# Performance work log

Hardware: AMD Instinct MI355X
Metric: run time of the kernel (lower is better)

## Reference

```python
import jax, jax.numpy as jnp
import numpy as np

B, Q, LE, D, P, A = 8, 32, 128, 512, 32, 128


def setup_inputs() -> dict:
    key = jax.random.key(0)
    ks = jax.random.split(key, 8)
    exp_tokens = jax.random.normal(ks[0], (B, Q, LE, D), dtype=jnp.float32)
    exp_mask = jax.random.randint(ks[1], (B, Q, LE), 0, 2, dtype=jnp.int32)
    s_j = jax.random.normal(ks[2], (B, P, D), dtype=jnp.float32)
    req_mask = jax.random.randint(ks[3], (B, P), 0, 2, dtype=jnp.int32)
    sc = 1.0 / np.sqrt(D)
    Ws_w = jax.random.normal(ks[4], (A, D), dtype=jnp.float32) * sc
    Ws_b = jax.random.normal(ks[5], (A,), dtype=jnp.float32) * 0.01
    U_w = jax.random.normal(ks[6], (A, D), dtype=jnp.float32) * sc
    v_w = jax.random.normal(ks[7], (1, A), dtype=jnp.float32) * (1.0 / np.sqrt(A))
    return {"exp_tokens": exp_tokens, "exp_mask": exp_mask, "s_j": s_j,
            "req_mask": req_mask, "Ws_w": Ws_w, "Ws_b": Ws_b, "U_w": U_w, "v_w": v_w}


def reference(exp_tokens, exp_mask, s_j, req_mask, Ws_w, Ws_b, U_w, v_w):
    # ws: (B,P,A); uh: (B,Q,Le,A)
    ws = jnp.einsum('bpd,ad->bpa', s_j, Ws_w) + Ws_b
    uh = jnp.einsum('bqtd,ad->bqta', exp_tokens, U_w)
    # broadcast add -> (B,Q,P,Le,A), tanh, project with v -> (B,Q,P,Le)
    scored = jnp.tanh(uh[:, :, None, :, :] + ws[:, None, :, None, :])
    e = jnp.einsum('bqpta,a->bqpt', scored, v_w[0])
    tok_mask = exp_mask[:, :, None, :]  # (B,Q,1,Le) broadcast over P
    e = jnp.where(tok_mask == 0, jnp.float32(-1e9), e)
    # joint softmax over Q*Le per (b,p)
    e_t = jnp.transpose(e, (0, 2, 1, 3)).reshape(e.shape[0], e.shape[2], -1)
    a = jax.nn.softmax(e_t, axis=-1).reshape(e.shape[0], e.shape[2], e.shape[1], e.shape[3])
    a = jnp.transpose(a, (0, 2, 1, 3))  # (B,Q,P,Le)
    s_rlk = jnp.einsum('bqpt,bqtd->bqpd', a, exp_tokens)
    rmask = req_mask[:, None, :, None].astype(s_rlk.dtype)
    return s_rlk * rmask
```

## Files before the change

### kernel.cpp

```cpp
#include <hip/hip_runtime.h>
#include <hip/hip_bf16.h>

#define B_  8
#define Q_  32
#define LE_ 128
#define D_  512
#define P_  32
#define A_  128

typedef __attribute__((ext_vector_type(8))) short short8_t;
typedef __attribute__((ext_vector_type(4))) float floatx4_t;

typedef const __attribute__((address_space(1))) unsigned int glb_uint;
typedef __attribute__((address_space(3))) unsigned int lds_uint;
#define GLD16(g, s) __builtin_amdgcn_global_load_lds((glb_uint*)(g), (lds_uint*)(s), 16, 0, 0)

__device__ __forceinline__ short f2bf(float x) {
    unsigned u = __float_as_uint(x);
    unsigned r = (u + 0x7fffu + ((u >> 16) & 1u)) >> 16;
    return (short)r;
}
__device__ __forceinline__ float bf2f(short s) {
    return __uint_as_float(((unsigned)(unsigned short)s) << 16);
}

__global__ __launch_bounds__(256) void convert_kernel(
    const float* __restrict__ X, const float* __restrict__ W,
    short* __restrict__ Xb, short* __restrict__ Wb) {
    int b = blockIdx.x;
    const float* src;
    short* dst;
    size_t base;
    if (b < 8192) {
        base = ((size_t)b * 256 + threadIdx.x) * 8;
        src = X + base; dst = Xb + base;
    } else {
        base = ((size_t)(b - 8192) * 256 + threadIdx.x) * 8;
        src = W + base; dst = Wb + base;
    }
    float4 v0 = ((const float4*)src)[0];
    float4 v1 = ((const float4*)src)[1];
    short8_t s;
    s[0] = f2bf(v0.x); s[1] = f2bf(v0.y); s[2] = f2bf(v0.z); s[3] = f2bf(v0.w);
    s[4] = f2bf(v1.x); s[5] = f2bf(v1.y); s[6] = f2bf(v1.z); s[7] = f2bf(v1.w);
    *(short8_t*)dst = s;
}

__global__ __launch_bounds__(128) void ws_kernel(
    const float* __restrict__ s_j, const float* __restrict__ Ws_w,
    const float* __restrict__ Ws_b, float* __restrict__ ws) {
    __shared__ float s_row[D_];
    int bp = blockIdx.x;
    const float* src = s_j + (size_t)bp * D_;
    for (int i = threadIdx.x; i < D_; i += 128) s_row[i] = src[i];
    __syncthreads();
    int a = threadIdx.x;
    const float4* w4 = (const float4*)(Ws_w + (size_t)a * D_);
    const float4* s4 = (const float4*)s_row;
    float acc = 0.0f;
#pragma unroll 8
    for (int i = 0; i < D_ / 4; ++i) {
        float4 w = w4[i];
        float4 s = s4[i];
        acc += w.x * s.x + w.y * s.y + w.z * s.z + w.w * s.w;
    }
    ws[bp * A_ + a] = __expf(2.0f * (acc + Ws_b[a]));
}

#define EUP_ 136
#define EWP_ 132
#define WPP_ 136

__global__ __launch_bounds__(512, 1) void score_kernel(
    const short* __restrict__ Xb, const short* __restrict__ Wb,
    const float* __restrict__ EW, const float* __restrict__ v_w,
    const int* __restrict__ exp_mask, float* __restrict__ gsums,
    short* __restrict__ wglob) {
    __shared__ short uA[128 * EUP_];
    __shared__ float ew_s[32 * EWP_];
    __shared__ short w_s[32 * WPP_];
    __shared__ float n2v[128];
    __shared__ int   mask_s[128];

    int bq = blockIdx.x;
    int b  = bq >> 5;
    int tid = threadIdx.x;
    int wave = tid >> 6, lane = tid & 63;
    int qd = lane >> 4, lr = lane & 15;

    short* As = uA;
    short* Bs = uA + 8192;

    int m0 = (wave >> 1) * 32, n0 = (wave & 1) * 64;
    int cA = lane & 7;
    int row0 = wave * 16 + (lane >> 3);

    floatx4_t acc[2][4];
#pragma unroll
    for (int i = 0; i < 2; ++i)
#pragma unroll
        for (int j = 0; j < 4; ++j) acc[i][j] = (floatx4_t){0.f, 0.f, 0.f, 0.f};

    for (int kt = 0; kt < 8; ++kt) {
        int k0 = kt * 64;
        __syncthreads();
#pragma unroll
        for (int u = 0; u < 2; ++u) {
            int m = row0 + u * 8;
            GLD16(Xb + (size_t)(bq * 128 + m) * D_ + k0 + ((cA ^ (m & 7)) * 8),
                  As + (wave * 2 + u) * 512);
        }
#pragma unroll
        for (int u = 0; u < 2; ++u) {
            int n = row0 + u * 8;
            GLD16(Wb + (size_t)n * D_ + k0 + ((cA ^ (n & 7)) * 8),
                  Bs + (wave * 2 + u) * 512);
        }
        __syncthreads();
#pragma unroll
        for (int ks = 0; ks < 2; ++ks) {
            int cr = (ks * 4 + qd) ^ (lr & 7);
            short8_t af[2], bfr[4];
#pragma unroll
            for (int i = 0; i < 2; ++i)
                af[i] = *(const short8_t*)(As + (m0 + i * 16 + lr) * 64 + cr * 8);
#pragma unroll
            for (int j = 0; j < 4; ++j)
                bfr[j] = *(const short8_t*)(Bs + (n0 + j * 16 + lr) * 64 + cr * 8);
#pragma unroll
            for (int i = 0; i < 2; ++i)
#pragma unroll
                for (int j = 0; j < 4; ++j)
                    acc[i][j] = __builtin_amdgcn_mfma_f32_16x16x32_bf16(af[i], bfr[j], acc[i][j], 0, 0, 0);
        }
    }
    __syncthreads();

#pragma unroll
    for (int i = 0; i < 2; ++i)
#pragma unroll
        for (int j = 0; j < 4; ++j)
#pragma unroll
            for (int r = 0; r < 4; ++r) {
                int t = m0 + i * 16 + qd * 4 + r;
                int a = n0 + j * 16 + lr;
                uA[t * EUP_ + a] = f2bf(__expf(2.0f * acc[i][j][r]));
            }
#pragma unroll
    for (int u = 0; u < 2; ++u) {
        int c = tid * 2 + u;
        int p = c >> 5, seg = c & 31;
        *(float4*)&ew_s[p * EWP_ + seg * 4] =
            *(const float4*)&EW[(size_t)(b * P_ + p) * A_ + seg * 4];
    }
    if (tid < 32) {
        float4 v = *(const float4*)(v_w + tid * 4);
        v.x *= -2.0f; v.y *= -2.0f; v.z *= -2.0f; v.w *= -2.0f;
        *(float4*)&n2v[tid * 4] = v;
    }
    if (tid < 128) mask_s[tid] = exp_mask[bq * LE_ + tid];
    __syncthreads();

    {
        int t = tid & 127, pg = tid >> 7;
        float acc8[8];
#pragma unroll
        for (int j = 0; j < 8; ++j) acc8[j] = 0.0f;
        for (int a8 = 0; a8 < 16; ++a8) {
            short8_t e8 = *(const short8_t*)&uA[t * EUP_ + a8 * 8];
            float eu[8];
#pragma unroll
            for (int k = 0; k < 8; ++k) eu[k] = bf2f(e8[k]);
            float4 nv0 = *(const float4*)&n2v[a8 * 8];
            float4 nv1 = *(const float4*)&n2v[a8 * 8 + 4];
            float nv[8] = {nv0.x, nv0.y, nv0.z, nv0.w, nv1.x, nv1.y, nv1.z, nv1.w};
#pragma unroll
            for (int j = 0; j < 8; ++j) {
                int p = pg * 8 + j;
                float4 w0 = *(const float4*)&ew_s[p * EWP_ + a8 * 8];
                float4 w1 = *(const float4*)&ew_s[p * EWP_ + a8 * 8 + 4];
                float ww[8] = {w0.x, w0.y, w0.z, w0.w, w1.x, w1.y, w1.z, w1.w};
#pragma unroll
                for (int k = 0; k < 8; ++k)
                    acc8[j] = fmaf(nv[k], __builtin_amdgcn_rcpf(fmaf(eu[k], ww[k], 1.0f)), acc8[j]);
            }
        }
        int mk = mask_s[t];
        short* wg = wglob + (size_t)bq * (P_ * LE_);
#pragma unroll
        for (int j = 0; j < 8; ++j) {
            float ee = mk ? __expf(acc8[j]) : 0.0f;
            short v = f2bf(ee);
            w_s[(pg * 8 + j) * WPP_ + t] = v;
            wg[(pg * 8 + j) * LE_ + t] = v;
        }
    }
    __syncthreads();

    if (tid < 256) {
        int p = tid >> 3, seg = tid & 7;
        const short* src = w_s + p * WPP_ + seg * 16;
        float s = 0.0f;
#pragma unroll
        for (int k = 0; k < 16; ++k) s += bf2f(src[k]);
        s += __shfl_xor(s, 1);
        s += __shfl_xor(s, 2);
        s += __shfl_xor(s, 4);
        if (seg == 0) atomicAdd(&gsums[b * P_ + p], s);
    }
}

__global__ __launch_bounds__(512, 4) void pv_kernel(
    const short* __restrict__ Xb, const short* __restrict__ wglob,
    const float* __restrict__ gsums, const int* __restrict__ req_mask,
    float* __restrict__ out) {
    __shared__ short pvB[128 * EUP_];
    __shared__ float rm_s[32];

    int blk = blockIdx.x;
    int bq = blk >> 2, chunk = blk & 3;
    int b = bq >> 5;
    int d0 = chunk * 128;
    int tid = threadIdx.x;
    int wave = tid >> 6, lane = tid & 63;
    int qd = lane >> 4, lr = lane & 15;

    if (tid < 32) {
        int bp = b * P_ + tid;
        float g = gsums[bp];
        rm_s[tid] = req_mask[bp] ? __builtin_amdgcn_rcpf(g) : 0.0f;
    }

    const short* wg = wglob + (size_t)bq * (P_ * LE_);
    short8_t afv[2][4];
#pragma unroll
    for (int i = 0; i < 2; ++i)
#pragma unroll
        for (int ks = 0; ks < 4; ++ks)
            afv[i][ks] = *(const short8_t*)&wg[(i * 16 + lr) * LE_ + ks * 32 + qd * 8];

    int tt = tid >> 2, dseg = (tid & 3) * 32;
    const short8_t* g = (const short8_t*)(Xb + (size_t)(bq * 128 + tt) * D_ + d0 + dseg);
    short8_t xs0 = g[0], xs1 = g[1], xs2 = g[2], xs3 = g[3];
#pragma unroll
    for (int e = 0; e < 8; ++e) {
        pvB[(dseg + 0 + e) * EUP_ + tt]  = xs0[e];
        pvB[(dseg + 8 + e) * EUP_ + tt]  = xs1[e];
        pvB[(dseg + 16 + e) * EUP_ + tt] = xs2[e];
        pvB[(dseg + 24 + e) * EUP_ + tt] = xs3[e];
    }
    __syncthreads();

    floatx4_t accp[2];
    accp[0] = (floatx4_t){0.f, 0.f, 0.f, 0.f};
    accp[1] = (floatx4_t){0.f, 0.f, 0.f, 0.f};
#pragma unroll
    for (int ks = 0; ks < 4; ++ks) {
        short8_t bfr = *(const short8_t*)&pvB[(wave * 16 + lr) * EUP_ + ks * 32 + qd * 8];
        accp[0] = __builtin_amdgcn_mfma_f32_16x16x32_bf16(afv[0][ks], bfr, accp[0], 0, 0, 0);
        accp[1] = __builtin_amdgcn_mfma_f32_16x16x32_bf16(afv[1][ks], bfr, accp[1], 0, 0, 0);
    }
#pragma unroll
    for (int i = 0; i < 2; ++i)
#pragma unroll
        for (int r = 0; r < 4; ++r) {
            int p = i * 16 + qd * 4 + r;
            __builtin_nontemporal_store(
                accp[i][r] * rm_s[p],
                &out[((size_t)bq * P_ + p) * D_ + d0 + wave * 16 + lr]);
        }
}

extern "C" void kernel_launch(void* const* d_in, const int* in_sizes, int n_in,
                              void* d_out, int out_size, void* d_ws, size_t ws_size,
                              hipStream_t stream) {
    const float* exp_tokens = (const float*)d_in[0];
    const int*   exp_mask   = (const int*)d_in[1];
    const float* s_j        = (const float*)d_in[2];
    const int*   req_mask   = (const int*)d_in[3];
    const float* Ws_w       = (const float*)d_in[4];
    const float* Ws_b       = (const float*)d_in[5];
    const float* U_w        = (const float*)d_in[6];
    const float* v_w        = (const float*)d_in[7];
    float* out = (float*)d_out;

    float* EW    = (float*)d_ws;
    float* gsums = EW + B_ * P_ * A_;
    short* Xb    = (short*)(gsums + 256);
    short* Wb    = Xb + (size_t)B_ * Q_ * LE_ * D_;
    short* wglob = Wb + (size_t)A_ * D_;

    hipMemsetAsync(gsums, 0, B_ * P_ * sizeof(float), stream);
    convert_kernel<<<dim3(8192 + 32), dim3(256), 0, stream>>>(exp_tokens, U_w, Xb, Wb);
    ws_kernel<<<dim3(B_ * P_), dim3(128), 0, stream>>>(s_j, Ws_w, Ws_b, EW);
    score_kernel<<<dim3(B_ * Q_), dim3(512), 0, stream>>>(Xb, Wb, EW, v_w, exp_mask, gsums, wglob);
    pv_kernel<<<dim3(B_ * Q_ * 4), dim3(512), 0, stream>>>(Xb, wglob, gsums, req_mask, out);
}
```

Before: 168.8 us.

## Split score kernel over token halves and fuse prep kernels

Merges the bf16 conversion, the Ws projection and the gsums zeroing into a single prep launch, which removes a memset and a separate launch. The score kernel now processes 64 tokens per block over twice as many blocks, with a higher launch_bounds occupancy target. The per-p sum is reduced with wave shuffles instead of an LDS staging pass. The trade-offs are recomputing the W tile loads per half and issuing more atomics.

```diff
diff --git a/kernel.cpp b/kernel.cpp
--- a/kernel.cpp
+++ b/kernel.cpp
@@ -24,95 +24,96 @@
     return __uint_as_float(((unsigned)(unsigned short)s) << 16);
 }
 
-__global__ __launch_bounds__(256) void convert_kernel(
+__global__ __launch_bounds__(256) void prep_kernel(
     const float* __restrict__ X, const float* __restrict__ W,
-    short* __restrict__ Xb, short* __restrict__ Wb) {
+    const float* __restrict__ s_j, const float* __restrict__ Ws_w,
+    const float* __restrict__ Ws_b,
+    short* __restrict__ Xb, short* __restrict__ Wb,
+    float* __restrict__ EW, float* __restrict__ gsums) {
+    __shared__ float s_row[D_];
     int b = blockIdx.x;
-    const float* src;
-    short* dst;
-    size_t base;
-    if (b < 8192) {
-        base = ((size_t)b * 256 + threadIdx.x) * 8;
-        src = X + base; dst = Xb + base;
-    } else {
-        base = ((size_t)(b - 8192) * 256 + threadIdx.x) * 8;
-        src = W + base; dst = Wb + base;
-    }
-    float4 v0 = ((const float4*)src)[0];
-    float4 v1 = ((const float4*)src)[1];
-    short8_t s;
-    s[0] = f2bf(v0.x); s[1] = f2bf(v0.y); s[2] = f2bf(v0.z); s[3] = f2bf(v0.w);
-    s[4] = f2bf(v1.x); s[5] = f2bf(v1.y); s[6] = f2bf(v1.z); s[7] = f2bf(v1.w);
-    *(short8_t*)dst = s;
-}
-
-__global__ __launch_bounds__(128) void ws_kernel(
-    const float* __restrict__ s_j, const float* __restrict__ Ws_w,
-    const float* __restrict__ Ws_b, float* __restrict__ ws) {
-    __shared__ float s_row[D_];
-    int bp = blockIdx.x;
+    int tid = threadIdx.x;
+    if (b < 8224) {
+        const float* src;
+        short* dst;
+        size_t base;
+        if (b < 8192) {
+            base = ((size_t)b * 256 + tid) * 8;
+            src = X + base; dst = Xb + base;
+        } else {
+            base = ((size_t)(b - 8192) * 256 + tid) * 8;
+            src = W + base; dst = Wb + base;
+        }
+        float4 v0 = ((const float4*)src)[0];
+        float4 v1 = ((const float4*)src)[1];
+        short8_t s;
+        s[0] = f2bf(v0.x); s[1] = f2bf(v0.y); s[2] = f2bf(v0.z); s[3] = f2bf(v0.w);
+        s[4] = f2bf(v1.x); s[5] = f2bf(v1.y); s[6] = f2bf(v1.z); s[7] = f2bf(v1.w);
+        *(short8_t*)dst = s;
+        return;
+    }
+    int bp = b - 8224;
+    if (b == 8224) gsums[tid] = 0.0f;
     const float* src = s_j + (size_t)bp * D_;
-    for (int i = threadIdx.x; i < D_; i += 128) s_row[i] = src[i];
-    __syncthreads();
-    int a = threadIdx.x;
-    const float4* w4 = (const float4*)(Ws_w + (size_t)a * D_);
-    const float4* s4 = (const float4*)s_row;
-    float acc = 0.0f;
+    for (int i = tid; i < D_; i += 256) s_row[i] = src[i];
+    __syncthreads();
+    if (tid < 128) {
+        int a = tid;
+        const float4* w4 = (const float4*)(Ws_w + (size_t)a * D_);
+        const float4* s4 = (const float4*)s_row;
+        float acc = 0.0f;
 #pragma unroll 8
-    for (int i = 0; i < D_ / 4; ++i) {
-        float4 w = w4[i];
-        float4 s = s4[i];
-        acc += w.x * s.x + w.y * s.y + w.z * s.z + w.w * s.w;
-    }
-    ws[bp * A_ + a] = __expf(2.0f * (acc + Ws_b[a]));
+        for (int i = 0; i < D_ / 4; ++i) {
+            float4 w = w4[i];
+            float s = w.x * s4[i].x + w.y * s4[i].y + w.z * s4[i].z + w.w * s4[i].w;
+            acc += s;
+        }
+        EW[bp * A_ + a] = __expf(2.0f * (acc + Ws_b[a]));
+    }
 }
 
 #define EUP_ 136
 #define EWP_ 132
-#define WPP_ 136
-
-__global__ __launch_bounds__(512, 1) void score_kernel(
+
+__global__ __launch_bounds__(512, 4) void score_kernel(
     const short* __restrict__ Xb, const short* __restrict__ Wb,
     const float* __restrict__ EW, const float* __restrict__ v_w,
     const int* __restrict__ exp_mask, float* __restrict__ gsums,
     short* __restrict__ wglob) {
-    __shared__ short uA[128 * EUP_];
+    __shared__ short uA[12288];
     __shared__ float ew_s[32 * EWP_];
-    __shared__ short w_s[32 * WPP_];
     __shared__ float n2v[128];
-    __shared__ int   mask_s[128];
-
-    int bq = blockIdx.x;
+    __shared__ int   mask_s[64];
+
+    int blk = blockIdx.x;
+    int bq = blk >> 1, t0 = (blk & 1) * 64;
     int b  = bq >> 5;
     int tid = threadIdx.x;
     int wave = tid >> 6, lane = tid & 63;
     int qd = lane >> 4, lr = lane & 15;
 
     short* As = uA;
-    short* Bs = uA + 8192;
-
-    int m0 = (wave >> 1) * 32, n0 = (wave & 1) * 64;
+    short* Bs = uA + 4096;
+
+    int m0 = (wave >> 2) * 32, n0 = (wave & 3) * 32;
     int cA = lane & 7;
-    int row0 = wave * 16 + (lane >> 3);
-
-    floatx4_t acc[2][4];
-#pragma unroll
-    for (int i = 0; i < 2; ++i)
-#pragma unroll
-        for (int j = 0; j < 4; ++j) acc[i][j] = (floatx4_t){0.f, 0.f, 0.f, 0.f};
+    int rowA  = wave * 8 + (lane >> 3);
+    int rowB0 = wave * 16 + (lane >> 3);
+
+    floatx4_t acc[2][2];
+#pragma unroll
+    for (int i = 0; i < 2; ++i)
+#pragma unroll
+        for (int j = 0; j < 2; ++j) acc[i][j] = (floatx4_t){0.f, 0.f, 0.f, 0.f};
 
     for (int kt = 0; kt < 8; ++kt) {
         int k0 = kt * 64;
         __syncthreads();
+        GLD16(Xb + (size_t)(bq * 128 + t0 + rowA) * D_ + k0 + ((cA ^ (rowA & 7)) * 8),
+              As + wave * 512);
 #pragma unroll
         for (int u = 0; u < 2; ++u) {
-            int m = row0 + u * 8;
-            GLD16(Xb + (size_t)(bq * 128 + m) * D_ + k0 + ((cA ^ (m & 7)) * 8),
-                  As + (wave * 2 + u) * 512);
-        }
-#pragma unroll
-        for (int u = 0; u < 2; ++u) {
-            int n = row0 + u * 8;
+            int n = rowB0 + u * 8;
             GLD16(Wb + (size_t)n * D_ + k0 + ((cA ^ (n & 7)) * 8),
                   Bs + (wave * 2 + u) * 512);
         }
@@ -120,17 +121,17 @@
 #pragma unroll
         for (int ks = 0; ks < 2; ++ks) {
             int cr = (ks * 4 + qd) ^ (lr & 7);
-            short8_t af[2], bfr[4];
+            short8_t af[2], bfr[2];
 #pragma unroll
             for (int i = 0; i < 2; ++i)
                 af[i] = *(const short8_t*)(As + (m0 + i * 16 + lr) * 64 + cr * 8);
 #pragma unroll
-            for (int j = 0; j < 4; ++j)
+            for (int j = 0; j < 2; ++j)
                 bfr[j] = *(const short8_t*)(Bs + (n0 + j * 16 + lr) * 64 + cr * 8);
 #pragma unroll
             for (int i = 0; i < 2; ++i)
 #pragma unroll
-                for (int j = 0; j < 4; ++j)
+                for (int j = 0; j < 2; ++j)
                     acc[i][j] = __builtin_amdgcn_mfma_f32_16x16x32_bf16(af[i], bfr[j], acc[i][j], 0, 0, 0);
         }
     }
@@ -139,7 +140,7 @@
 #pragma unroll
     for (int i = 0; i < 2; ++i)
 #pragma unroll
-        for (int j = 0; j < 4; ++j)
+        for (int j = 0; j < 2; ++j)
 #pragma unroll
             for (int r = 0; r < 4; ++r) {
                 int t = m0 + i * 16 + qd * 4 + r;
@@ -158,14 +159,14 @@
         v.x *= -2.0f; v.y *= -2.0f; v.z *= -2.0f; v.w *= -2.0f;
         *(float4*)&n2v[tid * 4] = v;
     }
-    if (tid < 128) mask_s[tid] = exp_mask[bq * LE_ + tid];
+    if (tid < 64) mask_s[tid] = exp_mask[bq * LE_ + t0 + tid];
     __syncthreads();
 
     {
-        int t = tid & 127, pg = tid >> 7;
-        float acc8[8];
-#pragma unroll
-        for (int j = 0; j < 8; ++j) acc8[j] = 0.0f;
+        int t = tid & 63, pg = tid >> 6;
+        float acc4[4];
+#pragma unroll
+        for (int j = 0; j < 4; ++j) acc4[j] = 0.0f;
         for (int a8 = 0; a8 < 16; ++a8) {
             short8_t e8 = *(const short8_t*)&uA[t * EUP_ + a8 * 8];
             float eu[8];
@@ -175,38 +176,37 @@
             float4 nv1 = *(const float4*)&n2v[a8 * 8 + 4];
             float nv[8] = {nv0.x, nv0.y, nv0.z, nv0.w, nv1.x, nv1.y, nv1.z, nv1.w};
 #pragma unroll
-            for (int j = 0; j < 8; ++j) {
-                int p = pg * 8 + j;
+            for (int j = 0; j < 4; ++j) {
+                int p = pg * 4 + j;
                 float4 w0 = *(const float4*)&ew_s[p * EWP_ + a8 * 8];
                 float4 w1 = *(const float4*)&ew_s[p * EWP_ + a8 * 8 + 4];
                 float ww[8] = {w0.x, w0.y, w0.z, w0.w, w1.x, w1.y, w1.z, w1.w};
 #pragma unroll
                 for (int k = 0; k < 8; ++k)
-                    acc8[j] = fmaf(nv[k], __builtin_amdgcn_rcpf(fmaf(eu[k], ww[k], 1.0f)), acc8[j]);
+                    acc4[j] = fmaf(nv[k], __builtin_amdgcn_rcpf(fmaf(eu[k], ww[k], 1.0f)), acc4[j]);
             }
         }
         int mk = mask_s[t];
         short* wg = wglob + (size_t)bq * (P_ * LE_);
-#pragma unroll
-        for (int j = 0; j < 8; ++j) {
-            float ee = mk ? __expf(acc8[j]) : 0.0f;
+        float sums[4];
+#pragma unroll
+        for (int j = 0; j < 4; ++j) {
+            float ee = mk ? __expf(acc4[j]) : 0.0f;
             short v = f2bf(ee);
-            w_s[(pg * 8 + j) * WPP_ + t] = v;
-            wg[(pg * 8 + j) * LE_ + t] = v;
-        }
-    }
-    __syncthreads();
-
-    if (tid < 256) {
-        int p = tid >> 3, seg = tid & 7;
-        const short* src = w_s + p * WPP_ + seg * 16;
-        float s = 0.0f;
-#pragma unroll
-        for (int k = 0; k < 16; ++k) s += bf2f(src[k]);
-        s += __shfl_xor(s, 1);
-        s += __shfl_xor(s, 2);
-        s += __shfl_xor(s, 4);
-        if (seg == 0) atomicAdd(&gsums[b * P_ + p], s);
+            wg[(pg * 4 + j) * LE_ + t0 + t] = v;
+            sums[j] = bf2f(v);
+        }
+#pragma unroll
+        for (int j = 0; j < 4; ++j) {
+            float s = sums[j];
+            s += __shfl_xor(s, 1);
+            s += __shfl_xor(s, 2);
+            s += __shfl_xor(s, 4);
+            s += __shfl_xor(s, 8);
+            s += __shfl_xor(s, 16);
+            s += __shfl_xor(s, 32);
+            if (lane == 0) atomicAdd(&gsums[b * P_ + pg * 4 + j], s);
+        }
     }
 }
 
@@ -290,9 +290,10 @@
     short* Wb    = Xb + (size_t)B_ * Q_ * LE_ * D_;
     short* wglob = Wb + (size_t)A_ * D_;
 
-    hipMemsetAsync(gsums, 0, B_ * P_ * sizeof(float), stream);
-    convert_kernel<<<dim3(8192 + 32), dim3(256), 0, stream>>>(exp_tokens, U_w, Xb, Wb);
-    ws_kernel<<<dim3(B_ * P_), dim3(128), 0, stream>>>(s_j, Ws_w, Ws_b, EW);
-    score_kernel<<<dim3(B_ * Q_), dim3(512), 0, stream>>>(Xb, Wb, EW, v_w, exp_mask, gsums, wglob);
-    pv_kernel<<<dim3(B_ * Q_ * 4), dim3(512), 0, stream>>>(Xb, wglob, gsums, req_mask, out);
-}
+    prep_kernel<<<dim3(8192 + 32 + 256), dim3(256), 0, stream>>>(
+        exp_tokens, U_w, s_j, Ws_w, Ws_b, Xb, Wb, EW, gsums);
+    score_kernel<<<dim3(B_ * Q_ * 2), dim3(512), 0, stream>>>(
+        Xb, Wb, EW, v_w, exp_mask, gsums, wglob);
+    pv_kernel<<<dim3(B_ * Q_ * 4), dim3(512), 0, stream>>>(
+        Xb, wglob, gsums, req_mask, out);
+}
```

Result: slower. 198.1 us (+17.4%).
